# Performance work log

Measured on AMD Instinct MI355X. Metric: run time of the kernel, lower is better.

The kernel has to match this reference:

```python
import jax, jax.numpy as jnp
import numpy as np

B, D, H = 65536, 64, 512  # batch, input_dim (even), hidden_dim; num_layers=4 -> 4 Linears


def setup_inputs() -> dict:
    key = jax.random.key(0)
    ks = jax.random.split(key, 10)
    s_in = 1.0 / np.sqrt(D)
    s_h = 1.0 / np.sqrt(H)
    return {
        "t": jnp.zeros((1,), jnp.float32),
        "x": jax.random.normal(ks[0], (B, D), jnp.float32),
        "W0": jax.random.uniform(ks[1], (D, H), jnp.float32, -s_in, s_in),
        "b0": jax.random.uniform(ks[2], (H,), jnp.float32, -s_in, s_in),
        "W1": jax.random.uniform(ks[3], (H, H), jnp.float32, -s_h, s_h),
        "b1": jax.random.uniform(ks[4], (H,), jnp.float32, -s_h, s_h),
        "W2": jax.random.uniform(ks[5], (H, H), jnp.float32, -s_h, s_h),
        "b2": jax.random.uniform(ks[6], (H,), jnp.float32, -s_h, s_h),
        "W3": jax.random.uniform(ks[7], (H, 1), jnp.float32, -s_h, s_h),
        "b3": jax.random.uniform(ks[8], (1,), jnp.float32, -s_h, s_h),
    }


def reference(t, x, W0, b0, W1, b1, W2, b2, W3, b3):
    # Hamiltonian MLP: Linear->Tanh x3, final Linear to scalar energy per sample.
    def hamiltonian_sum(xx):
        h = jnp.tanh(xx @ W0 + b0)
        h = jnp.tanh(h @ W1 + b1)
        h = jnp.tanh(h @ W2 + b2)
        return jnp.sum(h @ W3 + b3)

    gradH = jax.grad(hamiltonian_sum)(x)  # [B, D]
    n = D // 2
    # gradH @ J.T with symplectic J == concat(gradH_p, -gradH_q)
    return jnp.concatenate([gradH[:, n:], -gradH[:, :n]], axis=1)
```

## Files before the change

### kernel.cpp

```cpp
#include <hip/hip_runtime.h>
#include <hip/hip_bf16.h>

typedef unsigned short u16;
typedef short s16x8 __attribute__((ext_vector_type(8)));
typedef float f32x4 __attribute__((ext_vector_type(4)));

#define MFMA_BF16(a, b, c) __builtin_amdgcn_mfma_f32_16x16x32_bf16((a), (b), (c), 0, 0, 0)

static constexpr int D_IN   = 64;
static constexpr int H_DIM  = 512;
static constexpr int M_TILE = 64;
static constexpr int AST    = 520;
static constexpr int XST    = 72;

__device__ __forceinline__ u16 f2bf(float f) {
  unsigned u = __builtin_bit_cast(unsigned, f);
  u += 0x7fffu + ((u >> 16) & 1u);
  return (u16)(u >> 16);
}
__device__ __forceinline__ float bfb2f(unsigned bits16) {
  return __builtin_bit_cast(float, bits16 << 16);
}
__device__ __forceinline__ float fast_tanh(float x) {
  float e = __expf(2.0f * x);
  return 1.0f - 2.0f * __builtin_amdgcn_rcpf(e + 1.0f);
}

__global__ void prep_weights(const float* __restrict__ W0,
                             const float* __restrict__ W1,
                             const float* __restrict__ W2,
                             u16* __restrict__ ws) {
  u16* p0f = ws;
  u16* p0b = p0f + D_IN * H_DIM;
  u16* p1f = p0b + D_IN * H_DIM;
  u16* p1b = p1f + H_DIM * H_DIM;
  u16* p2f = p1b + H_DIM * H_DIM;
  u16* p2b = p2f + H_DIM * H_DIM;

  int t = blockIdx.x * 256 + threadIdx.x;
  int lane = t & 63;
  int kc   = (t >> 6) & 15;
  int ntg  = t >> 10;
  int ln = lane & 15, q = lane >> 4;
  int n = ntg * 16 + ln;
  int k = kc * 32 + q * 8;

  #pragma unroll
  for (int j = 0; j < 8; ++j) {
    p1f[t * 8 + j] = f2bf(W1[(k + j) * 512 + n]);
    p2f[t * 8 + j] = f2bf(W2[(k + j) * 512 + n]);
    p1b[t * 8 + j] = f2bf(W1[n * 512 + (k + j)]);
    p2b[t * 8 + j] = f2bf(W2[n * 512 + (k + j)]);
  }
  if (kc < 2) {
    int t0 = (ntg * 2 + kc) * 64 + lane;
    #pragma unroll
    for (int j = 0; j < 8; ++j)
      p0f[t0 * 8 + j] = f2bf(W0[(k + j) * 512 + n]);
  }
  if (ntg < 4) {
    int t0 = (ntg * 16 + kc) * 64 + lane;
    #pragma unroll
    for (int j = 0; j < 8; ++j)
      p0b[t0 * 8 + j] = f2bf(W0[n * 512 + (k + j)]);
  }
}

#define LOAD_B4(BP, KC, BR)                                                     \
  {                                                                             \
    const u16* _sr = (BP) + ((size_t)wave << 15) + ((KC) << 9) + lane * 8;      \
    _Pragma("unroll")                                                           \
    for (int s = 0; s < 4; ++s)                                                 \
      (BR)[s] = *(const s16x8*)(_sr + (s << 13));                               \
  }

#define GEMM512_REG(BP)                                                         \
  {                                                                             \
    _Pragma("unroll") for (int mt = 0; mt < 4; ++mt)                            \
      _Pragma("unroll") for (int nt = 0; nt < 4; ++nt)                          \
        acc[mt][nt] = (f32x4){0.f, 0.f, 0.f, 0.f};                              \
    for (int kc2 = 0; kc2 < 8; ++kc2) {                                         \
      const int e = kc2 * 2;                                                    \
      {                                                                         \
        s16x8 a[4];                                                             \
        _Pragma("unroll")                                                       \
        for (int mt = 0; mt < 4; ++mt)                                          \
          a[mt] = *(const s16x8*)(buf + (mt * 16 + ln) * AST + e * 32 + q * 8); \
        _Pragma("unroll")                                                       \
        for (int nt = 0; nt < 4; ++nt)                                          \
          _Pragma("unroll")                                                     \
          for (int mt = 0; mt < 4; ++mt)                                        \
            acc[mt][nt] = MFMA_BF16(a[mt], bregA[nt], acc[mt][nt]);             \
        if (kc2 < 7) LOAD_B4(BP, e + 2, bregA);                                 \
      }                                                                         \
      const int o = e + 1;                                                      \
      {                                                                         \
        s16x8 a[4];                                                             \
        _Pragma("unroll")                                                       \
        for (int mt = 0; mt < 4; ++mt)                                          \
          a[mt] = *(const s16x8*)(buf + (mt * 16 + ln) * AST + o * 32 + q * 8); \
        _Pragma("unroll")                                                       \
        for (int nt = 0; nt < 4; ++nt)                                          \
          _Pragma("unroll")                                                     \
          for (int mt = 0; mt < 4; ++mt)                                        \
            acc[mt][nt] = MFMA_BF16(a[mt], bregB[nt], acc[mt][nt]);             \
        if (kc2 < 7) LOAD_B4(BP, o + 2, bregB);                                 \
      }                                                                         \
    }                                                                           \
  }

__global__ __launch_bounds__(512, 2) void hnn_fused(
    const float* __restrict__ x,
    const float* __restrict__ bias0,
    const float* __restrict__ bias1,
    const float* __restrict__ bias2,
    const float* __restrict__ W3,
    const u16* __restrict__ ws,
    float* __restrict__ out)
{
  const u16* p0f = ws;
  const u16* p0b = p0f + D_IN * H_DIM;
  const u16* p1f = p0b + D_IN * H_DIM;
  const u16* p1b = p1f + H_DIM * H_DIM;
  const u16* p2f = p1b + H_DIM * H_DIM;
  const u16* p2b = p2f + H_DIM * H_DIM;

  __shared__ __align__(16) u16 xs[M_TILE * XST];
  __shared__ __align__(16) u16 buf[M_TILE * AST];

  const int tid  = threadIdx.x;
  const int wave = tid >> 6;
  const int lane = tid & 63;
  const int ln   = lane & 15;
  const int q    = lane >> 4;
  const int nwb  = wave * 64;
  const int row0 = blockIdx.x * M_TILE;

  {
    int r = tid >> 3, c = (tid & 7) * 8;
    const float4* src = (const float4*)(x + (size_t)(row0 + r) * D_IN + c);
    float4 f0 = src[0];
    float4 f1 = src[1];
    u16* dst = xs + r * XST + c;
    dst[0] = f2bf(f0.x); dst[1] = f2bf(f0.y); dst[2] = f2bf(f0.z); dst[3] = f2bf(f0.w);
    dst[4] = f2bf(f1.x); dst[5] = f2bf(f1.y); dst[6] = f2bf(f1.z); dst[7] = f2bf(f1.w);
  }
  __syncthreads();

  f32x4 acc[4][4];
  s16x8 bregA[4], bregB[4];
  unsigned h0p[4][4][2];
  unsigned h1p[4][4][2];
  float bias[4];

  #pragma unroll
  for (int nt = 0; nt < 4; ++nt) bias[nt] = bias0[nwb + nt * 16 + ln];
  #pragma unroll
  for (int mt = 0; mt < 4; ++mt)
    #pragma unroll
    for (int nt = 0; nt < 4; ++nt) acc[mt][nt] = (f32x4){0.f, 0.f, 0.f, 0.f};
  {
    const u16* bpw0 = p0f + (wave << 12) + lane * 8;
    #pragma unroll
    for (int kc = 0; kc < 2; ++kc) {
      s16x8 a[4];
      #pragma unroll
      for (int mt = 0; mt < 4; ++mt)
        a[mt] = *(const s16x8*)(xs + (mt * 16 + ln) * XST + kc * 32 + q * 8);
      #pragma unroll
      for (int nt = 0; nt < 4; ++nt) {
        s16x8 b = *(const s16x8*)(bpw0 + (nt << 10) + (kc << 9));
        #pragma unroll
        for (int mt = 0; mt < 4; ++mt)
          acc[mt][nt] = MFMA_BF16(a[mt], b, acc[mt][nt]);
      }
    }
  }
  LOAD_B4(p1f, 0, bregA);
  LOAD_B4(p1f, 1, bregB);
  #pragma unroll
  for (int mt = 0; mt < 4; ++mt)
    #pragma unroll
    for (int nt = 0; nt < 4; ++nt) {
      int col = nwb + nt * 16 + ln;
      u16 u[4];
      #pragma unroll
      for (int r = 0; r < 4; ++r) {
        float th = fast_tanh(acc[mt][nt][r] + bias[nt]);
        u[r] = f2bf(th);
        buf[(mt * 16 + q * 4 + r) * AST + col] = u[r];
      }
      h0p[mt][nt][0] = (unsigned)u[0] | ((unsigned)u[1] << 16);
      h0p[mt][nt][1] = (unsigned)u[2] | ((unsigned)u[3] << 16);
    }
  __syncthreads();

  #pragma unroll
  for (int nt = 0; nt < 4; ++nt) bias[nt] = bias1[nwb + nt * 16 + ln];
  GEMM512_REG(p1f);
  __syncthreads();
  LOAD_B4(p2f, 0, bregA);
  LOAD_B4(p2f, 1, bregB);
  #pragma unroll
  for (int mt = 0; mt < 4; ++mt)
    #pragma unroll
    for (int nt = 0; nt < 4; ++nt) {
      int col = nwb + nt * 16 + ln;
      u16 u[4];
      #pragma unroll
      for (int r = 0; r < 4; ++r) {
        float th = fast_tanh(acc[mt][nt][r] + bias[nt]);
        u[r] = f2bf(th);
        buf[(mt * 16 + q * 4 + r) * AST + col] = u[r];
      }
      h1p[mt][nt][0] = (unsigned)u[0] | ((unsigned)u[1] << 16);
      h1p[mt][nt][1] = (unsigned)u[2] | ((unsigned)u[3] << 16);
    }
  __syncthreads();

  #pragma unroll
  for (int nt = 0; nt < 4; ++nt) bias[nt] = bias2[nwb + nt * 16 + ln];
  float w3v[4];
  #pragma unroll
  for (int nt = 0; nt < 4; ++nt) w3v[nt] = W3[nwb + nt * 16 + ln];
  GEMM512_REG(p2f);
  __syncthreads();
  LOAD_B4(p2b, 0, bregA);
  LOAD_B4(p2b, 1, bregB);
  #pragma unroll
  for (int mt = 0; mt < 4; ++mt)
    #pragma unroll
    for (int nt = 0; nt < 4; ++nt) {
      int col = nwb + nt * 16 + ln;
      #pragma unroll
      for (int r = 0; r < 4; ++r) {
        float th = fast_tanh(acc[mt][nt][r] + bias[nt]);
        float gz = w3v[nt] * (1.0f - th * th);
        buf[(mt * 16 + q * 4 + r) * AST + col] = f2bf(gz);
      }
    }
  __syncthreads();

  GEMM512_REG(p2b);
  __syncthreads();
  LOAD_B4(p1b, 0, bregA);
  LOAD_B4(p1b, 1, bregB);
  #pragma unroll
  for (int mt = 0; mt < 4; ++mt)
    #pragma unroll
    for (int nt = 0; nt < 4; ++nt) {
      int col = nwb + nt * 16 + ln;
      unsigned pa = h1p[mt][nt][0], pb = h1p[mt][nt][1];
      float hh[4] = { bfb2f(pa & 0xffffu), bfb2f(pa >> 16),
                      bfb2f(pb & 0xffffu), bfb2f(pb >> 16) };
      #pragma unroll
      for (int r = 0; r < 4; ++r) {
        float gz = acc[mt][nt][r] * (1.0f - hh[r] * hh[r]);
        buf[(mt * 16 + q * 4 + r) * AST + col] = f2bf(gz);
      }
    }
  __syncthreads();

  GEMM512_REG(p1b);
  __syncthreads();
  #pragma unroll
  for (int mt = 0; mt < 4; ++mt)
    #pragma unroll
    for (int nt = 0; nt < 4; ++nt) {
      int col = nwb + nt * 16 + ln;
      unsigned pa = h0p[mt][nt][0], pb = h0p[mt][nt][1];
      float hh[4] = { bfb2f(pa & 0xffffu), bfb2f(pa >> 16),
                      bfb2f(pb & 0xffffu), bfb2f(pb >> 16) };
      #pragma unroll
      for (int r = 0; r < 4; ++r) {
        float gz = acc[mt][nt][r] * (1.0f - hh[r] * hh[r]);
        buf[(mt * 16 + q * 4 + r) * AST + col] = f2bf(gz);
      }
    }
  __syncthreads();

  {
    f32x4 acc5[2];
    acc5[0] = (f32x4){0.f, 0.f, 0.f, 0.f};
    acc5[1] = (f32x4){0.f, 0.f, 0.f, 0.f};
    const int mt5 = wave & 3;
    const int nb5 = (wave >> 2) * 32;
    const u16* bp5 = p0b + ((wave >> 2) << 14) + lane * 8;
    #pragma unroll 2
    for (int kc = 0; kc < 16; ++kc) {
      s16x8 a = *(const s16x8*)(buf + (mt5 * 16 + ln) * AST + kc * 32 + q * 8);
      #pragma unroll
      for (int nt = 0; nt < 2; ++nt) {
        s16x8 b = *(const s16x8*)(bp5 + (nt << 13) + (kc << 9));
        acc5[nt] = MFMA_BF16(a, b, acc5[nt]);
      }
    }
    #pragma unroll
    for (int nt = 0; nt < 2; ++nt) {
      int g = nb5 + nt * 16 + ln;
      int c = (g < 32) ? g + 32 : g - 32;
      float s = (g < 32) ? -1.0f : 1.0f;
      #pragma unroll
      for (int r = 0; r < 4; ++r) {
        int grow = row0 + mt5 * 16 + q * 4 + r;
        out[(size_t)grow * 64 + c] = s * acc5[nt][r];
      }
    }
  }
}

extern "C" void kernel_launch(void* const* d_in, const int* in_sizes, int n_in,
                              void* d_out, int out_size, void* d_ws, size_t ws_size,
                              hipStream_t stream) {
  const float* x  = (const float*)d_in[1];
  const float* W0 = (const float*)d_in[2];
  const float* b0 = (const float*)d_in[3];
  const float* W1 = (const float*)d_in[4];
  const float* b1 = (const float*)d_in[5];
  const float* W2 = (const float*)d_in[6];
  const float* b2 = (const float*)d_in[7];
  const float* W3 = (const float*)d_in[8];
  u16* ws = (u16*)d_ws;
  float* out = (float*)d_out;

  prep_weights<<<128, 256, 0, stream>>>(W0, W1, W2, ws);
  hnn_fused<<<65536 / M_TILE, 512, 0, stream>>>(x, b0, b1, b2, W3, ws, out);
}
```

Baseline: 227.4 us.

## Deepen GEMM pipeline to four B register stages and double-buffer A fragments

Replaces the two-stage B register prefetch in each 512-wide GEMM with a four-stage ring (bb0..bb3) and double-buffers the LDS A fragments, so global weight loads are issued four k-chunks ahead and LDS reads one chunk ahead. It also aliases the x staging buffer onto the main LDS buffer, adding a sync after layer 0, to cut shared memory use. The cost is higher VGPR pressure (16 B vectors plus 8 A vectors live alongside 64 accumulators and saved activations), which at launch bounds 512x2 risks spills.

```diff
diff --git a/kernel.cpp b/kernel.cpp
--- a/kernel.cpp
+++ b/kernel.cpp
@@ -66,47 +66,60 @@
   }
 }
 
-#define LOAD_B4(BP, KC, BR)                                                     \
+#define LOAD_A2(DST, KC)                                                        \
+  _Pragma("unroll")                                                             \
+  for (int mt = 0; mt < 4; ++mt)                                                \
+    (DST)[mt] = *(const s16x8*)(buf + (mt * 16 + ln) * AST + (KC) * 32 + q * 8);
+
+#define LOAD_B4P(BP, KC, BB)                                                    \
   {                                                                             \
     const u16* _sr = (BP) + ((size_t)wave << 15) + ((KC) << 9) + lane * 8;      \
     _Pragma("unroll")                                                           \
     for (int s = 0; s < 4; ++s)                                                 \
-      (BR)[s] = *(const s16x8*)(_sr + (s << 13));                               \
-  }
-
-#define GEMM512_REG(BP)                                                         \
+      (BB)[s] = *(const s16x8*)(_sr + (s << 13));                               \
+  }
+#define BB_PROLOGUE(BP)                                                         \
+  { LOAD_B4P(BP, 0, bb0); LOAD_B4P(BP, 1, bb1);                                 \
+    LOAD_B4P(BP, 2, bb2); LOAD_B4P(BP, 3, bb3); }
+
+#define PIPE_STEP(KC, PAR, BB, BP)                                              \
+  {                                                                             \
+    LOAD_A2(a[((PAR) + 1) & 1], (KC) + 1);                                      \
+    _Pragma("unroll")                                                           \
+    for (int nt = 0; nt < 4; ++nt)                                              \
+      _Pragma("unroll")                                                         \
+      for (int mt = 0; mt < 4; ++mt)                                            \
+        acc[mt][nt] = MFMA_BF16(a[(PAR) & 1][mt], (BB)[nt], acc[mt][nt]);       \
+    LOAD_B4P(BP, (KC) + 4, BB);                                                 \
+  }
+#define PIPE_TAIL(KC, PAR, BB, LOADA)                                           \
+  {                                                                             \
+    if (LOADA) LOAD_A2(a[((PAR) + 1) & 1], (KC) + 1);                           \
+    _Pragma("unroll")                                                           \
+    for (int nt = 0; nt < 4; ++nt)                                              \
+      _Pragma("unroll")                                                         \
+      for (int mt = 0; mt < 4; ++mt)                                            \
+        acc[mt][nt] = MFMA_BF16(a[(PAR) & 1][mt], (BB)[nt], acc[mt][nt]);       \
+  }
+
+#define GEMM512_PIPE(BP)                                                        \
   {                                                                             \
     _Pragma("unroll") for (int mt = 0; mt < 4; ++mt)                            \
       _Pragma("unroll") for (int nt = 0; nt < 4; ++nt)                          \
         acc[mt][nt] = (f32x4){0.f, 0.f, 0.f, 0.f};                              \
-    for (int kc2 = 0; kc2 < 8; ++kc2) {                                         \
-      const int e = kc2 * 2;                                                    \
-      {                                                                         \
-        s16x8 a[4];                                                             \
-        _Pragma("unroll")                                                       \
-        for (int mt = 0; mt < 4; ++mt)                                          \
-          a[mt] = *(const s16x8*)(buf + (mt * 16 + ln) * AST + e * 32 + q * 8); \
-        _Pragma("unroll")                                                       \
-        for (int nt = 0; nt < 4; ++nt)                                          \
-          _Pragma("unroll")                                                     \
-          for (int mt = 0; mt < 4; ++mt)                                        \
-            acc[mt][nt] = MFMA_BF16(a[mt], bregA[nt], acc[mt][nt]);             \
-        if (kc2 < 7) LOAD_B4(BP, e + 2, bregA);                                 \
-      }                                                                         \
-      const int o = e + 1;                                                      \
-      {                                                                         \
-        s16x8 a[4];                                                             \
-        _Pragma("unroll")                                                       \
-        for (int mt = 0; mt < 4; ++mt)                                          \
-          a[mt] = *(const s16x8*)(buf + (mt * 16 + ln) * AST + o * 32 + q * 8); \
-        _Pragma("unroll")                                                       \
-        for (int nt = 0; nt < 4; ++nt)                                          \
-          _Pragma("unroll")                                                     \
-          for (int mt = 0; mt < 4; ++mt)                                        \
-            acc[mt][nt] = MFMA_BF16(a[mt], bregB[nt], acc[mt][nt]);             \
-        if (kc2 < 7) LOAD_B4(BP, o + 2, bregB);                                 \
-      }                                                                         \
+    s16x8 a[2][4];                                                              \
+    LOAD_A2(a[0], 0);                                                           \
+    for (int kb = 0; kb < 3; ++kb) {                \
+      const int k0 = kb * 4;                                                    \
+      PIPE_STEP(k0 + 0, 0, bb0, BP);                                            \
+      PIPE_STEP(k0 + 1, 1, bb1, BP);                                            \
+      PIPE_STEP(k0 + 2, 2, bb2, BP);                                            \
+      PIPE_STEP(k0 + 3, 3, bb3, BP);                                            \
     }                                                                           \
+    PIPE_TAIL(12, 0, bb0, 1);                             \
+    PIPE_TAIL(13, 1, bb1, 1);                                                   \
+    PIPE_TAIL(14, 0, bb2, 1);                                                   \
+    PIPE_TAIL(15, 1, bb3, 0);                                                   \
   }
 
 __global__ __launch_bounds__(512, 2) void hnn_fused(
@@ -125,8 +138,8 @@
   const u16* p2f = p1b + H_DIM * H_DIM;
   const u16* p2b = p2f + H_DIM * H_DIM;
 
-  __shared__ __align__(16) u16 xs[M_TILE * XST];
   __shared__ __align__(16) u16 buf[M_TILE * AST];
+  u16* xs = buf;
 
   const int tid  = threadIdx.x;
   const int wave = tid >> 6;
@@ -148,7 +161,7 @@
   __syncthreads();
 
   f32x4 acc[4][4];
-  s16x8 bregA[4], bregB[4];
+  s16x8 bb0[4], bb1[4], bb2[4], bb3[4];
   unsigned h0p[4][4][2];
   unsigned h1p[4][4][2];
   float bias[4];
@@ -163,21 +176,21 @@
     const u16* bpw0 = p0f + (wave << 12) + lane * 8;
     #pragma unroll
     for (int kc = 0; kc < 2; ++kc) {
-      s16x8 a[4];
+      s16x8 a0[4];
       #pragma unroll
       for (int mt = 0; mt < 4; ++mt)
-        a[mt] = *(const s16x8*)(xs + (mt * 16 + ln) * XST + kc * 32 + q * 8);
+        a0[mt] = *(const s16x8*)(xs + (mt * 16 + ln) * XST + kc * 32 + q * 8);
       #pragma unroll
       for (int nt = 0; nt < 4; ++nt) {
         s16x8 b = *(const s16x8*)(bpw0 + (nt << 10) + (kc << 9));
         #pragma unroll
         for (int mt = 0; mt < 4; ++mt)
-          acc[mt][nt] = MFMA_BF16(a[mt], b, acc[mt][nt]);
-      }
-    }
-  }
-  LOAD_B4(p1f, 0, bregA);
-  LOAD_B4(p1f, 1, bregB);
+          acc[mt][nt] = MFMA_BF16(a0[mt], b, acc[mt][nt]);
+      }
+    }
+  }
+  __syncthreads();
+  BB_PROLOGUE(p1f);
   #pragma unroll
   for (int mt = 0; mt < 4; ++mt)
     #pragma unroll
@@ -197,10 +210,9 @@
 
   #pragma unroll
   for (int nt = 0; nt < 4; ++nt) bias[nt] = bias1[nwb + nt * 16 + ln];
-  GEMM512_REG(p1f);
-  __syncthreads();
-  LOAD_B4(p2f, 0, bregA);
-  LOAD_B4(p2f, 1, bregB);
+  GEMM512_PIPE(p1f);
+  __syncthreads();
+  BB_PROLOGUE(p2f);
   #pragma unroll
   for (int mt = 0; mt < 4; ++mt)
     #pragma unroll
@@ -223,10 +235,9 @@
   float w3v[4];
   #pragma unroll
   for (int nt = 0; nt < 4; ++nt) w3v[nt] = W3[nwb + nt * 16 + ln];
-  GEMM512_REG(p2f);
-  __syncthreads();
-  LOAD_B4(p2b, 0, bregA);
-  LOAD_B4(p2b, 1, bregB);
+  GEMM512_PIPE(p2f);
+  __syncthreads();
+  BB_PROLOGUE(p2b);
   #pragma unroll
   for (int mt = 0; mt < 4; ++mt)
     #pragma unroll
@@ -241,10 +252,9 @@
     }
   __syncthreads();
 
-  GEMM512_REG(p2b);
-  __syncthreads();
-  LOAD_B4(p1b, 0, bregA);
-  LOAD_B4(p1b, 1, bregB);
+  GEMM512_PIPE(p2b);
+  __syncthreads();
+  BB_PROLOGUE(p1b);
   #pragma unroll
   for (int mt = 0; mt < 4; ++mt)
     #pragma unroll
@@ -261,7 +271,7 @@
     }
   __syncthreads();
 
-  GEMM512_REG(p1b);
+  GEMM512_PIPE(p1b);
   __syncthreads();
   #pragma unroll
   for (int mt = 0; mt < 4; ++mt)
@@ -288,11 +298,11 @@
     const u16* bp5 = p0b + ((wave >> 2) << 14) + lane * 8;
     #pragma unroll 2
     for (int kc = 0; kc < 16; ++kc) {
-      s16x8 a = *(const s16x8*)(buf + (mt5 * 16 + ln) * AST + kc * 32 + q * 8);
+      s16x8 a5 = *(const s16x8*)(buf + (mt5 * 16 + ln) * AST + kc * 32 + q * 8);
       #pragma unroll
       for (int nt = 0; nt < 2; ++nt) {
         s16x8 b = *(const s16x8*)(bp5 + (nt << 13) + (kc << 9));
-        acc5[nt] = MFMA_BF16(a, b, acc5[nt]);
+        acc5[nt] = MFMA_BF16(a5, b, acc5[nt]);
       }
     }
     #pragma unroll
```

Measured after the change: 383.8 us. 1.69x slower.
